# Optimization experiments

Measured on AMD Instinct MI355X. Metric: run time of the kernel, lower is better.

The kernel has to match this reference:

```python
import jax, jax.numpy as jnp
import numpy as np

N_EMBD = 1024
N_HEAD = 16
HEAD_DIM = N_EMBD // N_HEAD


def setup_inputs() -> dict:
    key = jax.random.key(0)
    k1, k2, k3 = jax.random.split(key, 3)
    B, T, C = 2, 2048, N_EMBD
    x = jax.random.normal(k1, (B, T, C), dtype=jnp.float32)
    # torch nn.Linear(n_embd, 3*n_embd): weight [3C, C], bias [3C]
    W = jax.random.normal(k2, (3 * C, C), dtype=jnp.float32) * (1.0 / np.sqrt(C))
    b = jax.random.normal(k3, (3 * C,), dtype=jnp.float32) * 0.01
    return {"x": x, "W": W, "b": b}


def reference(x, W, b):
    B, T, C = x.shape
    H, D = N_HEAD, HEAD_DIM
    qkv = jnp.einsum('btc,oc->bto', x, W) + b          # [B,T,3C]
    q, k, v = jnp.split(qkv, 3, axis=2)
    # [B,H,T,D]
    q = q.reshape(B, T, H, D).transpose(0, 2, 1, 3)
    k = k.reshape(B, T, H, D).transpose(0, 2, 1, 3)
    v = v.reshape(B, T, H, D).transpose(0, 2, 1, 3)
    scale = 1.0 / np.sqrt(D).astype(np.float32)
    scores = jnp.einsum('bhid,bhjd->bhij', q, k) * scale   # [B,H,T,T]
    causal = jnp.tril(jnp.ones((T, T), dtype=bool))
    w = jnp.where(causal, jax.nn.relu(scores), 0.0)        # ReLU, no softmax
    y = jnp.einsum('bhij,bhjd->bhid', w, v)                # [B,H,T,D]
    return y.transpose(0, 2, 1, 3).reshape(B, T, C)
```

## Files before the change

kernel.cpp:

```cpp
#include <hip/hip_runtime.h>

typedef __bf16 bf16;
typedef __bf16 bf16x8 __attribute__((ext_vector_type(8)));
typedef float  f32x4  __attribute__((ext_vector_type(4)));

#define T_SEQ   2048
#define D_HEAD  64
#define NH      16
#define BH      32
#define C_EMB   1024
#define WS_STRIDE (BH * T_SEQ * D_HEAD)
#define XN (4096 * 1024)
#define WN (3072 * 1024)
#define WS_NEEDED ((size_t)(3 * WS_STRIDE + XN + WN) * 2)
#define CVT_GRID 3584

__device__ __forceinline__ bf16x8 cvt8(float4 a, float4 b) {
    bf16x8 r;
    r[0] = (__bf16)a.x; r[1] = (__bf16)a.y; r[2] = (__bf16)a.z; r[3] = (__bf16)a.w;
    r[4] = (__bf16)b.x; r[5] = (__bf16)b.y; r[6] = (__bf16)b.z; r[7] = (__bf16)b.w;
    return r;
}

__device__ __forceinline__ void gl_lds16(const bf16* g, bf16* l) {
    __builtin_amdgcn_global_load_lds(
        (const __attribute__((address_space(1))) unsigned int*)g,
        (__attribute__((address_space(3))) unsigned int*)l,
        16, 0, 0);
}

__device__ __forceinline__ unsigned pack_bf16(float a, float b) {
    union { __bf16 h[2]; unsigned u; } pk;
    pk.h[0] = (__bf16)a; pk.h[1] = (__bf16)b;
    return pk.u;
}

__global__ __launch_bounds__(256) void cvt_bf16(
    const float* __restrict__ x, const float* __restrict__ W,
    bf16* __restrict__ xb, bf16* __restrict__ wb)
{
    const int t = blockIdx.x * 256 + threadIdx.x;
    const float* src; bf16* dst; int base;
    if (t < XN / 8) { src = x; dst = xb; base = t * 8; }
    else           { src = W; dst = wb; base = (t - XN / 8) * 8; }
    float4 a = *(const float4*)(src + base);
    float4 b = *(const float4*)(src + base + 4);
    *(bf16x8*)(dst + base) = cvt8(a, b);
}

#define LDA(d, qi) {                                                          \
    const bf16* abase_ = Sh + (d)*16384 + (qi)*8192 + (wm*64 + l15)*64;       \
    _Pragma("unroll")                                                         \
    for (int ii_ = 0; ii_ < 4; ii_++) {                                       \
        _Pragma("unroll")                                                     \
        for (int dk_ = 0; dk_ < 2; dk_++)                                     \
            aF[ii_][dk_] = *(const bf16x8*)(abase_ + ii_*1024                 \
                                            + (((dk_*4 + l4) ^ k7) * 8));     \
    }                                                                         \
}

#define LDB(d, qj, bFv) {                                                     \
    const bf16* bbase_ = Sh + 32768 + (d)*16384 + (qj)*8192                   \
                         + (wn*32 + l15)*64;                                  \
    _Pragma("unroll")                                                         \
    for (int jj_ = 0; jj_ < 2; jj_++) {                                       \
        _Pragma("unroll")                                                     \
        for (int dk_ = 0; dk_ < 2; dk_++)                                     \
            bFv[jj_][dk_] = *(const bf16x8*)(bbase_ + jj_*1024                \
                                             + (((dk_*4 + l4) ^ k7) * 8));    \
    }                                                                         \
}

#define STA(d, qi, s, ko) gl_lds16(                                           \
    aSrc + (size_t)((qi)*64 + (s)*128) * 1024 + (ko),                         \
    Sh + (d)*16384 + (qi)*8192 + (s)*4096 + w*512)

#define STB(d, qj, s, ko) gl_lds16(                                           \
    bSrc + (size_t)((s)*128 + (qj)*32) * 1024 + (ko),                         \
    Sh + 32768 + (d)*16384 + (qj)*8192 + (s)*4096 + w*512)

#define MMAQ(qi, qj, bFv) {                                                   \
    __builtin_amdgcn_s_setprio(1);                                            \
    _Pragma("unroll")                                                         \
    for (int dk_ = 0; dk_ < 2; dk_++) {                                       \
        _Pragma("unroll")                                                     \
        for (int ii_ = 0; ii_ < 4; ii_++) {                                   \
            _Pragma("unroll")                                                 \
            for (int jj_ = 0; jj_ < 2; jj_++)                                 \
                acc[(qi)*4 + ii_][(qj)*2 + jj_] =                             \
                    __builtin_amdgcn_mfma_f32_16x16x32_bf16(                  \
                        aF[ii_][dk_], bFv[jj_][dk_],                          \
                        acc[(qi)*4 + ii_][(qj)*2 + jj_], 0, 0, 0);            \
        }                                                                     \
    }                                                                         \
    __builtin_amdgcn_s_setprio(0);                                            \
}

#define BAR   __builtin_amdgcn_s_barrier()
#define LGKM0 asm volatile("s_waitcnt lgkmcnt(0)" ::: "memory")

#define HALF(d, sk)                                                           \
                                                                      \
    LDA(d, 0) LDB(d, 0, bF0)                                                  \
    BAR; LGKM0;                                                               \
    MMAQ(0, 0, bF0)                                                           \
    BAR;                                                                      \
                                                                      \
    LDB(d, 1, bF1)                                                            \
    STA(d, 0, 0, sk); STA(d, 0, 1, sk); STB(d, 0, 0, sk); STB(d, 0, 1, sk);   \
    BAR; LGKM0;                                                               \
    MMAQ(0, 1, bF1)                                                           \
    BAR;                                                                      \
                                                                      \
    LDA(d, 1)                                                                 \
    STB(d, 1, 0, sk); STB(d, 1, 1, sk);                                       \
    BAR; LGKM0;                                                               \
    MMAQ(1, 0, bF0)                                                           \
    BAR;                                                                      \
                                                                      \
    STA(d, 1, 0, sk); STA(d, 1, 1, sk);                                       \
    BAR;                                                                      \
    MMAQ(1, 1, bF1)                                                           \
    asm volatile("s_waitcnt vmcnt(8)" ::: "memory");                          \
    BAR;

__global__ __launch_bounds__(512, 2) void qkv_gemm3(
    const bf16* __restrict__ xb, const bf16* __restrict__ wb,
    const float* __restrict__ bias, bf16* __restrict__ ws)
{
    __shared__ bf16 Sh[65536];

    const int tid  = threadIdx.x;
    const int lane = tid & 63;
    const int w    = tid >> 6;
    const int wm   = w >> 2, wn = w & 3;
    const int l15  = lane & 15, l4 = lane >> 4;
    const int k7   = l15 & 7;
    const int l8   = lane >> 3;
    const int csw  = (lane & 7) ^ l8;

    const int swz = (blockIdx.x & 7) * 24 + (blockIdx.x >> 3);
    const int bm  = swz / 12, bn = swz % 12;

    const bf16* aSrc = xb + (size_t)(bm * 256 + w * 8 + l8) * 1024 + csw * 8;
    const bf16* bSrc = wb + (size_t)(bn * 256 + (w >> 2) * 64 + (w & 3) * 8 + l8) * 1024
                          + csw * 8;

    f32x4 acc[8][4];
#pragma unroll
    for (int i = 0; i < 8; i++)
#pragma unroll
        for (int j = 0; j < 4; j++) acc[i][j] = (f32x4){0.f, 0.f, 0.f, 0.f};

    bf16x8 aF[4][2], bF0[2][2], bF1[2][2];

    STA(0,0,0,0);  STA(0,0,1,0);  STB(0,0,0,0);  STB(0,0,1,0);
    STB(0,1,0,0);  STB(0,1,1,0);  STA(0,1,0,0);  STA(0,1,1,0);
    STA(1,0,0,64); STA(1,0,1,64); STB(1,0,0,64); STB(1,0,1,64);
    STB(1,1,0,64); STB(1,1,1,64); STA(1,1,0,64); STA(1,1,1,64);
    asm volatile("s_waitcnt vmcnt(8)" ::: "memory");
    BAR;

    for (int it = 0; it < 8; ++it) {
        const int sk0 = (it < 7 ? (2 * it + 2) : 15) * 64;
        const int sk1 = (it < 7 ? (2 * it + 3) : 15) * 64;
        HALF(0, sk0)
        HALF(1, sk1)
    }
    asm volatile("s_waitcnt vmcnt(0)" ::: "memory");
    BAR;

    float bv[4];
#pragma unroll
    for (int j = 0; j < 4; j++) bv[j] = bias[bn * 256 + wn * 64 + j * 16 + l15];

    const int which = bn >> 2;
    const int h     = (bn & 3) * 4 + wn;
    const int bi    = bm >> 3;
    const int tBase = (bm & 7) * 256 + wm * 128;
    const float qs  = (which == 0) ? 0.125f : 1.0f;
    bf16* Wl = Sh + w * 8192;

    if (which < 2) {
#pragma unroll
        for (int i = 0; i < 8; i++)
#pragma unroll
            for (int j = 0; j < 4; j++)
#pragma unroll
                for (int r = 0; r < 4; r++) {
                    const int lm = i * 16 + l4 * 4 + r;
                    const int dd = j * 16 + l15;
                    const int cp = (dd >> 3) ^ (lm & 7);
                    Wl[lm * 64 + cp * 8 + (dd & 7)] =
                        (__bf16)((acc[i][j][r] + bv[j]) * qs);
                }
#pragma unroll
        for (int e = 0; e < 16; e++) {
            const int lm = e * 8 + l8;
            const int c  = lane & 7;
            bf16x8 v8 = *(const bf16x8*)&Wl[lm * 64 + ((c ^ (lm & 7)) * 8)];
            const int t = tBase + lm;
            *(bf16x8*)&ws[(size_t)which * WS_STRIDE
                          + ((size_t)(bi * NH + h) * T_SEQ + t) * D_HEAD + c * 8] = v8;
        }
    } else {
#pragma unroll
        for (int i = 0; i < 8; i++)
#pragma unroll
            for (int j = 0; j < 4; j++) {
                const int dd = j * 16 + l15;
#pragma unroll
                for (int p = 0; p < 2; p++) {
                    const int lm = i * 16 + l4 * 4 + 2 * p;
                    const int ch = lm >> 3;
                    const int cp = (ch & 8) | ((ch & 7) ^ (dd & 7));
                    *(unsigned*)&Wl[dd * 128 + cp * 8 + (lm & 7)] =
                        pack_bf16(acc[i][j][2 * p] + bv[j],
                                  acc[i][j][2 * p + 1] + bv[j]);
                }
            }
        bf16* vt = ws + 2 * (size_t)WS_STRIDE;
#pragma unroll
        for (int e = 0; e < 16; e++) {
            const int dd = e * 4 + l4;
            const int c  = l15;
            const int cp = (c & 8) | ((c & 7) ^ (dd & 7));
            bf16x8 v8 = *(const bf16x8*)&Wl[dd * 128 + cp * 8];
            *(bf16x8*)&vt[((size_t)(bi * NH + h) * D_HEAD + dd) * T_SEQ
                          + tBase + c * 8] = v8;
        }
    }
}

__global__ __launch_bounds__(256) void qkv_gemm(
    const float* __restrict__ x, const float* __restrict__ W,
    const float* __restrict__ bias, bf16* __restrict__ ws)
{
    __shared__ bf16 As[128 * 40];
    __shared__ bf16 Bs[128 * 40];

    const int tid  = threadIdx.x;
    const int lane = tid & 63;
    const int w    = tid >> 6;
    const int wm   = w >> 1, wn = w & 1;
    const int l15  = lane & 15, l4 = lane >> 4;
    const int bm   = blockIdx.x / 24, bn = blockIdx.x % 24;

    const int srow = tid >> 1;
    const int scol = (tid & 1) * 16;
    const float* xg = x + (size_t)(bm * 128 + srow) * 1024 + scol;
    const float* wg = W + (size_t)(bn * 128 + srow) * 1024 + scol;
    bf16* asw = &As[srow * 40 + scol];
    bf16* bsw = &Bs[srow * 40 + scol];

    f32x4 acc[4][4];
#pragma unroll
    for (int i = 0; i < 4; i++)
#pragma unroll
        for (int j = 0; j < 4; j++) acc[i][j] = (f32x4){0.f, 0.f, 0.f, 0.f};

    float bv[4];
#pragma unroll
    for (int j = 0; j < 4; j++) bv[j] = bias[bn * 128 + wn * 64 + j * 16 + l15];

    for (int kk = 0; kk < 32; ++kk) {
        const float* xp = xg + kk * 32;
        const float* wp = wg + kk * 32;
        float4 a0 = *(const float4*)(xp + 0);
        float4 a1 = *(const float4*)(xp + 4);
        float4 a2 = *(const float4*)(xp + 8);
        float4 a3 = *(const float4*)(xp + 12);
        float4 b0 = *(const float4*)(wp + 0);
        float4 b1 = *(const float4*)(wp + 4);
        float4 b2 = *(const float4*)(wp + 8);
        float4 b3 = *(const float4*)(wp + 12);

        __syncthreads();
        *(bf16x8*)(asw + 0) = cvt8(a0, a1);
        *(bf16x8*)(asw + 8) = cvt8(a2, a3);
        *(bf16x8*)(bsw + 0) = cvt8(b0, b1);
        *(bf16x8*)(bsw + 8) = cvt8(b2, b3);
        __syncthreads();

        bf16x8 aF[4], bF[4];
#pragma unroll
        for (int s = 0; s < 4; s++) {
            aF[s] = *(const bf16x8*)&As[(wm * 64 + s * 16 + l15) * 40 + l4 * 8];
            bF[s] = *(const bf16x8*)&Bs[(wn * 64 + s * 16 + l15) * 40 + l4 * 8];
        }
#pragma unroll
        for (int i = 0; i < 4; i++)
#pragma unroll
            for (int j = 0; j < 4; j++)
                acc[i][j] = __builtin_amdgcn_mfma_f32_16x16x32_bf16(
                    aF[i], bF[j], acc[i][j], 0, 0, 0);
    }

#pragma unroll
    for (int i = 0; i < 4; i++) {
#pragma unroll
        for (int j = 0; j < 4; j++) {
            const int n     = bn * 128 + wn * 64 + j * 16 + l15;
            const int which = n >> 10;
            const int cc    = n & 1023;
            const int h     = cc >> 6, d = cc & 63;
            const float qs  = (which == 0) ? 0.125f : 1.0f;
#pragma unroll
            for (int r = 0; r < 4; r++) {
                const int m  = bm * 128 + wm * 64 + i * 16 + l4 * 4 + r;
                const int bi = m >> 11, t = m & 2047;
                const int bh = bi * NH + h;
                const float v = (acc[i][j][r] + bv[j]) * qs;
                size_t idx;
                if (which == 2)
                    idx = 2 * (size_t)WS_STRIDE + ((size_t)bh * D_HEAD + d) * T_SEQ + t;
                else
                    idx = (size_t)which * WS_STRIDE + ((size_t)bh * T_SEQ + t) * D_HEAD + d;
                ws[idx] = (__bf16)v;
            }
        }
    }
}

#define ASTAGE(jt_, p_) {                                                     \
    _Pragma("unroll")                                                         \
    for (int e_ = 0; e_ < 4; e_++) {                                          \
        const int rb_ = w * 32 + e_ * 8;                                      \
        gl_lds16(kg + (size_t)((jt_) * 128 + rb_ + ksub) * 64                 \
                    + ((kc ^ ksub) * 8),                                      \
                 &Ks[p_][rb_ * 64]);                                          \
    }                                                                         \
    _Pragma("unroll")                                                         \
    for (int e_ = 0; e_ < 4; e_++) {                                          \
        const int rb_ = w * 16 + e_ * 4;                                      \
        const int sw_ = (rb_ & 12) + vsub;                                    \
        gl_lds16(vt + (size_t)(rb_ + vsub) * T_SEQ + (jt_) * 128              \
                    + ((vc ^ sw_) * 8),                                       \
                 &Vts[p_][rb_ * 128]);                                        \
    }                                                                         \
}

__global__ __launch_bounds__(256) void attn(
    const bf16* __restrict__ ws, float* __restrict__ out)
{
    __shared__ bf16 Ks[2][128 * 64];
    __shared__ bf16 Vts[2][64 * 128];

    const int tid  = threadIdx.x;
    const int lane = tid & 63;
    const int w    = tid >> 6;
    const int l15  = lane & 15, qd = lane >> 4;

    const int bh = blockIdx.x & 31;
    const int u  = blockIdx.x >> 5;
    const int qt = (u < 8) ? u : (23 - u);
    const int nj = qt + 1;
    const int qb = qt * 128;

    const bf16* qg = ws + (size_t)bh * (T_SEQ * D_HEAD);
    const bf16* kg = ws + WS_STRIDE + (size_t)bh * (T_SEQ * D_HEAD);
    const bf16* vt = ws + 2 * (size_t)WS_STRIDE + (size_t)bh * (D_HEAD * T_SEQ);
    const int b = bh >> 4, h = bh & 15;

    const int ksub = lane >> 3;
    const int kc   = lane & 7;
    const int vsub = qd;
    const int vc   = l15;

    bf16x8 qF[2][2];
#pragma unroll
    for (int sm = 0; sm < 2; sm++)
#pragma unroll
        for (int dk = 0; dk < 2; dk++)
            qF[sm][dk] = *(const bf16x8*)(qg
                + (qb + w * 32 + sm * 16 + l15) * 64 + dk * 32 + qd * 8);

    f32x4 o[2][4];
#pragma unroll
    for (int sm = 0; sm < 2; sm++)
#pragma unroll
        for (int sd = 0; sd < 4; sd++) o[sm][sd] = (f32x4){0.f, 0.f, 0.f, 0.f};

    ASTAGE(0, 0);

    for (int jt = 0; jt < nj; ++jt) {
        const int p = jt & 1;
        if (jt + 1 < nj) {
            ASTAGE(jt + 1, p ^ 1);
            asm volatile("s_waitcnt vmcnt(8)" ::: "memory");
        } else {
            asm volatile("s_waitcnt vmcnt(0)" ::: "memory");
        }
        BAR;

        const bf16* Kp = Ks[p];
        const bf16* Vp = Vts[p];

        const bool need_mask = (jt == nj - 1);
        unsigned PK[2][8][2];
#pragma unroll
        for (int kn = 0; kn < 8; kn++) {
            const int r7  = 4 * (kn & 1) + (l15 & 3);
            const int row = 32 * (kn >> 1) + 8 * (l15 >> 2) + r7;
            bf16x8 kf0 = *(const bf16x8*)&Kp[row * 64 + ((qd ^ r7) * 8)];
            bf16x8 kf1 = *(const bf16x8*)&Kp[row * 64 + (((4 + qd) ^ r7) * 8)];
            f32x4 s0 = {0.f, 0.f, 0.f, 0.f}, s1 = {0.f, 0.f, 0.f, 0.f};
            __builtin_amdgcn_s_setprio(1);
            s0 = __builtin_amdgcn_mfma_f32_16x16x32_bf16(kf0, qF[0][0], s0, 0, 0, 0);
            s0 = __builtin_amdgcn_mfma_f32_16x16x32_bf16(kf1, qF[0][1], s0, 0, 0, 0);
            s1 = __builtin_amdgcn_mfma_f32_16x16x32_bf16(kf0, qF[1][0], s1, 0, 0, 0);
            s1 = __builtin_amdgcn_mfma_f32_16x16x32_bf16(kf1, qF[1][1], s1, 0, 0, 0);
            __builtin_amdgcn_s_setprio(0);
            const int keyb = jt * 128 + 32 * (kn >> 1) + 8 * qd + 4 * (kn & 1);
#pragma unroll
            for (int sm = 0; sm < 2; sm++) {
                const f32x4 sv = sm ? s1 : s0;
                float v[4];
#pragma unroll
                for (int r = 0; r < 4; r++) v[r] = fmaxf(sv[r], 0.f);
                if (need_mask) {
                    const int q = qb + w * 32 + sm * 16 + l15;
#pragma unroll
                    for (int r = 0; r < 4; r++)
                        if (q < keyb + r) v[r] = 0.f;
                }
                PK[sm][kn][0] = pack_bf16(v[0], v[1]);
                PK[sm][kn][1] = pack_bf16(v[2], v[3]);
            }
        }

#pragma unroll
        for (int kk = 0; kk < 4; kk++) {
            bf16x8 pF[2];
#pragma unroll
            for (int sm = 0; sm < 2; sm++) {
                union { unsigned dw[4]; bf16x8 v; } uu;
                uu.dw[0] = PK[sm][2 * kk + 0][0];
                uu.dw[1] = PK[sm][2 * kk + 0][1];
                uu.dw[2] = PK[sm][2 * kk + 1][0];
                uu.dw[3] = PK[sm][2 * kk + 1][1];
                pF[sm] = uu.v;
            }
            __builtin_amdgcn_s_setprio(1);
#pragma unroll
            for (int sd = 0; sd < 4; sd++) {
                bf16x8 vf = *(const bf16x8*)&Vp[(sd * 16 + l15) * 128
                                                + (((kk * 4 + qd) ^ l15) * 8)];
                o[0][sd] = __builtin_amdgcn_mfma_f32_16x16x32_bf16(pF[0], vf, o[0][sd], 0, 0, 0);
                o[1][sd] = __builtin_amdgcn_mfma_f32_16x16x32_bf16(pF[1], vf, o[1][sd], 0, 0, 0);
            }
            __builtin_amdgcn_s_setprio(0);
        }

        BAR;
    }

#pragma unroll
    for (int sm = 0; sm < 2; sm++)
#pragma unroll
        for (int sd = 0; sd < 4; sd++) {
            const int d = sd * 16 + l15;
#pragma unroll
            for (int r = 0; r < 4; r++) {
                const int t = qb + w * 32 + sm * 16 + qd * 4 + r;
                out[((size_t)b * T_SEQ + t) * C_EMB + h * 64 + d] = o[sm][sd][r];
            }
        }
}

extern "C" void kernel_launch(void* const* d_in, const int* in_sizes, int n_in,
                              void* d_out, int out_size, void* d_ws, size_t ws_size,
                              hipStream_t stream) {
    const float* x    = (const float*)d_in[0];
    const float* W    = (const float*)d_in[1];
    const float* bias = (const float*)d_in[2];
    float* out        = (float*)d_out;
    bf16*  ws         = (bf16*)d_ws;

    if (ws_size >= WS_NEEDED) {
        bf16* xb = ws + 3 * (size_t)WS_STRIDE;
        bf16* wb = xb + XN;
        cvt_bf16<<<dim3(CVT_GRID), dim3(256), 0, stream>>>(x, W, xb, wb);
        qkv_gemm3<<<dim3(192), dim3(512), 0, stream>>>(xb, wb, bias, ws);
    } else {
        qkv_gemm<<<dim3(768), dim3(256), 0, stream>>>(x, W, bias, ws);
    }
    attn<<<dim3(512), dim3(256), 0, stream>>>(ws, out);
}
```

Measured before the change: 146.7 us.

## Single-buffer V tile, loaded per iteration and overlapped with QK^T compute

V staging is split from K staging. V is now single-buffered and issued at the start of each iteration, so its load overlaps the score MFMAs, with an extra wait and barrier placed before the PV stage. K rows get a new XOR swizzle with precomputed per-lane offsets, and each load of four K fragments is reused across two key sub-blocks. This halves V's LDS footprint, which may allow higher occupancy, but adds a barrier per iteration and exposes V load latency if the score phase is short.

Result: no change. 147.2 us (+0.4%).

```diff
diff --git a/kernel.cpp b/kernel.cpp
--- a/kernel.cpp
+++ b/kernel.cpp
@@ -322,29 +322,32 @@
     }
 }
 
-#define ASTAGE(jt_, p_) {                                                     \
+#define KSTAGE(jt_, p_) {                                                     \
     _Pragma("unroll")                                                         \
     for (int e_ = 0; e_ < 4; e_++) {                                          \
         const int rb_ = w * 32 + e_ * 8;                                      \
         gl_lds16(kg + (size_t)((jt_) * 128 + rb_ + ksub) * 64                 \
-                    + ((kc ^ ksub) * 8),                                      \
-                 &Ks[p_][rb_ * 64]);                                          \
+                    + ((kc ^ ksub ^ (e_ << 1)) * 8),                          \
+                 &Kb[p_][rb_ * 64]);                                          \
     }                                                                         \
+}
+
+#define VSTAGE(jt_) {                                                         \
     _Pragma("unroll")                                                         \
     for (int e_ = 0; e_ < 4; e_++) {                                          \
         const int rb_ = w * 16 + e_ * 4;                                      \
-        const int sw_ = (rb_ & 12) + vsub;                                    \
+        const int sw_ = (rb_ & 12) + vsub;                 \
         gl_lds16(vt + (size_t)(rb_ + vsub) * T_SEQ + (jt_) * 128              \
                     + ((vc ^ sw_) * 8),                                       \
-                 &Vts[p_][rb_ * 128]);                                        \
+                 &Vts[rb_ * 128]);                                            \
     }                                                                         \
 }
 
 __global__ __launch_bounds__(256) void attn(
     const bf16* __restrict__ ws, float* __restrict__ out)
 {
-    __shared__ bf16 Ks[2][128 * 64];
-    __shared__ bf16 Vts[2][64 * 128];
+    __shared__ bf16 Kb[2][128 * 64];
+    __shared__ bf16 Vts[64 * 128];
 
     const int tid  = threadIdx.x;
     const int lane = tid & 63;
@@ -367,6 +370,11 @@
     const int vsub = qd;
     const int vc   = l15;
 
+    const int krow0 = 8 * (l15 >> 2) + (l15 & 3);
+    const int pos00 = qd ^ (l15 & 3) ^ ((l15 >> 2) << 1);
+    const int kbO0  = krow0 * 64 + pos00 * 8;
+    const int kbO1  = krow0 * 64 + (pos00 ^ 4) * 8;
+
     bf16x8 qF[2][2];
 #pragma unroll
     for (int sm = 0; sm < 2; sm++)
@@ -381,53 +389,64 @@
 #pragma unroll
         for (int sd = 0; sd < 4; sd++) o[sm][sd] = (f32x4){0.f, 0.f, 0.f, 0.f};
 
-    ASTAGE(0, 0);
+    KSTAGE(0, 0);
 
     for (int jt = 0; jt < nj; ++jt) {
         const int p = jt & 1;
-        if (jt + 1 < nj) {
-            ASTAGE(jt + 1, p ^ 1);
+        const bool more = (jt + 1 < nj);
+        VSTAGE(jt);
+        if (more) {
+            KSTAGE(jt + 1, p ^ 1);
             asm volatile("s_waitcnt vmcnt(8)" ::: "memory");
         } else {
-            asm volatile("s_waitcnt vmcnt(0)" ::: "memory");
+            asm volatile("s_waitcnt vmcnt(4)" ::: "memory");
         }
         BAR;
 
-        const bf16* Kp = Ks[p];
-        const bf16* Vp = Vts[p];
+        const bf16* kb0 = &Kb[p][kbO0];
+        const bf16* kb1 = &Kb[p][kbO1];
 
         const bool need_mask = (jt == nj - 1);
         unsigned PK[2][8][2];
 #pragma unroll
-        for (int kn = 0; kn < 8; kn++) {
-            const int r7  = 4 * (kn & 1) + (l15 & 3);
-            const int row = 32 * (kn >> 1) + 8 * (l15 >> 2) + r7;
-            bf16x8 kf0 = *(const bf16x8*)&Kp[row * 64 + ((qd ^ r7) * 8)];
-            bf16x8 kf1 = *(const bf16x8*)&Kp[row * 64 + (((4 + qd) ^ r7) * 8)];
-            f32x4 s0 = {0.f, 0.f, 0.f, 0.f}, s1 = {0.f, 0.f, 0.f, 0.f};
-            __builtin_amdgcn_s_setprio(1);
-            s0 = __builtin_amdgcn_mfma_f32_16x16x32_bf16(kf0, qF[0][0], s0, 0, 0, 0);
-            s0 = __builtin_amdgcn_mfma_f32_16x16x32_bf16(kf1, qF[0][1], s0, 0, 0, 0);
-            s1 = __builtin_amdgcn_mfma_f32_16x16x32_bf16(kf0, qF[1][0], s1, 0, 0, 0);
-            s1 = __builtin_amdgcn_mfma_f32_16x16x32_bf16(kf1, qF[1][1], s1, 0, 0, 0);
-            __builtin_amdgcn_s_setprio(0);
-            const int keyb = jt * 128 + 32 * (kn >> 1) + 8 * qd + 4 * (kn & 1);
-#pragma unroll
-            for (int sm = 0; sm < 2; sm++) {
-                const f32x4 sv = sm ? s1 : s0;
-                float v[4];
-#pragma unroll
-                for (int r = 0; r < 4; r++) v[r] = fmaxf(sv[r], 0.f);
-                if (need_mask) {
-                    const int q = qb + w * 32 + sm * 16 + l15;
-#pragma unroll
-                    for (int r = 0; r < 4; r++)
-                        if (q < keyb + r) v[r] = 0.f;
+        for (int m = 0; m < 4; m++) {
+            bf16x8 kf[2][2];
+            kf[0][0] = *(const bf16x8*)(kb0 + m * 2048);
+            kf[0][1] = *(const bf16x8*)(kb1 + m * 2048);
+            kf[1][0] = *(const bf16x8*)(kb1 + m * 2048 + 256);
+            kf[1][1] = *(const bf16x8*)(kb0 + m * 2048 + 256);
+#pragma unroll
+            for (int h2 = 0; h2 < 2; h2++) {
+                const int kn = 2 * m + h2;
+                f32x4 s0 = {0.f, 0.f, 0.f, 0.f}, s1 = {0.f, 0.f, 0.f, 0.f};
+                __builtin_amdgcn_s_setprio(1);
+                s0 = __builtin_amdgcn_mfma_f32_16x16x32_bf16(kf[h2][0], qF[0][0], s0, 0, 0, 0);
+                s0 = __builtin_amdgcn_mfma_f32_16x16x32_bf16(kf[h2][1], qF[0][1], s0, 0, 0, 0);
+                s1 = __builtin_amdgcn_mfma_f32_16x16x32_bf16(kf[h2][0], qF[1][0], s1, 0, 0, 0);
+                s1 = __builtin_amdgcn_mfma_f32_16x16x32_bf16(kf[h2][1], qF[1][1], s1, 0, 0, 0);
+                __builtin_amdgcn_s_setprio(0);
+                const int keyb = jt * 128 + 32 * m + 8 * qd + 4 * h2;
+#pragma unroll
+                for (int sm = 0; sm < 2; sm++) {
+                    const f32x4 sv = sm ? s1 : s0;
+                    float v[4];
+#pragma unroll
+                    for (int r = 0; r < 4; r++) v[r] = fmaxf(sv[r], 0.f);
+                    if (need_mask) {
+                        const int q = qb + w * 32 + sm * 16 + l15;
+#pragma unroll
+                        for (int r = 0; r < 4; r++)
+                            if (q < keyb + r) v[r] = 0.f;
+                    }
+                    PK[sm][kn][0] = pack_bf16(v[0], v[1]);
+                    PK[sm][kn][1] = pack_bf16(v[2], v[3]);
                 }
-                PK[sm][kn][0] = pack_bf16(v[0], v[1]);
-                PK[sm][kn][1] = pack_bf16(v[2], v[3]);
             }
         }
+
+        if (more) asm volatile("s_waitcnt vmcnt(4)" ::: "memory");
+        else      asm volatile("s_waitcnt vmcnt(0)" ::: "memory");
+        BAR;
 
 #pragma unroll
         for (int kk = 0; kk < 4; kk++) {
@@ -444,8 +463,8 @@
             __builtin_amdgcn_s_setprio(1);
 #pragma unroll
             for (int sd = 0; sd < 4; sd++) {
-                bf16x8 vf = *(const bf16x8*)&Vp[(sd * 16 + l15) * 128
-                                                + (((kk * 4 + qd) ^ l15) * 8)];
+                bf16x8 vf = *(const bf16x8*)&Vts[(sd * 16 + l15) * 128
+                                                 + (((kk * 4 + qd) ^ l15) * 8)];
                 o[0][sd] = __builtin_amdgcn_mfma_f32_16x16x32_bf16(pF[0], vf, o[0][sd], 0, 0, 0);
                 o[1][sd] = __builtin_amdgcn_mfma_f32_16x16x32_bf16(pF[1], vf, o[1][sd], 0, 0, 0);
             }
```
